# Optimization experiments

Measured on AMD Instinct MI355X. Metric: run time of the kernel, lower is better.

## Reference

```python
import jax, jax.numpy as jnp
import numpy as np

N, E, G = 40000, 400000, 64
IN, ED, HID, HEADS, OUT = 2, 18, 64, 4, 3

def _glorot(key, shape):
    fan_in = shape[0]
    return jax.random.normal(key, shape, dtype=jnp.float32) / np.float32(np.sqrt(fan_in))

def setup_inputs():
    key = jax.random.key(0)
    ks = jax.random.split(key, 32)
    d1 = HEADS * HID  # 256
    return {
        "x": jax.random.normal(ks[0], (N, IN), jnp.float32),
        "edge_index": jax.random.randint(ks[1], (2, E), 0, N),
        "edge_attr": jax.random.normal(ks[2], (E, ED), jnp.float32),
        "batch": jnp.sort(jax.random.randint(ks[3], (N,), 0, G)),
        # conv1: TransformerConv(2 -> 64, heads=4, concat=True, beta=True, edge_dim=18)
        "Wq1": _glorot(ks[4], (IN, d1)), "bq1": jnp.zeros((d1,), jnp.float32),
        "Wk1": _glorot(ks[5], (IN, d1)), "bk1": jnp.zeros((d1,), jnp.float32),
        "Wv1": _glorot(ks[6], (IN, d1)), "bv1": jnp.zeros((d1,), jnp.float32),
        "We1": _glorot(ks[7], (ED, d1)),
        "Wskip1": _glorot(ks[8], (IN, d1)), "bskip1": jnp.zeros((d1,), jnp.float32),
        "Wbeta1": _glorot(ks[9], (3 * d1, 1)),
        # conv2: TransformerConv(256 -> 64, heads=1, concat=False, beta=True, edge_dim=18)
        "Wq2": _glorot(ks[10], (d1, HID)), "bq2": jnp.zeros((HID,), jnp.float32),
        "Wk2": _glorot(ks[11], (d1, HID)), "bk2": jnp.zeros((HID,), jnp.float32),
        "Wv2": _glorot(ks[12], (d1, HID)), "bv2": jnp.zeros((HID,), jnp.float32),
        "We2": _glorot(ks[13], (ED, HID)),
        "Wskip2": _glorot(ks[14], (d1, HID)), "bskip2": jnp.zeros((HID,), jnp.float32),
        "Wbeta2": _glorot(ks[15], (3 * HID, 1)),
        "Wlin": _glorot(ks[16], (HID, OUT)), "blin": jnp.zeros((OUT,), jnp.float32),
    }

def _tconv(x, src, dst, edge_attr, Wq, bq, Wk, bk, Wv, bv, We, Wskip, bskip, Wbeta, H, C, concat):
    # PyG TransformerConv with edge_dim, beta=True, root_weight=True (eval: dropout off)
    n = x.shape[0]
    q = (x @ Wq + bq).reshape(n, H, C)
    k = (x @ Wk + bk).reshape(n, H, C)
    v = (x @ Wv + bv).reshape(n, H, C)
    e = (edge_attr @ We).reshape(-1, H, C)              # [E,H,C]
    kj = k[src] + e                                      # key_j + edge
    alpha = jnp.einsum('ehc,ehc->eh', q[dst], kj) * (1.0 / (C ** 0.5))  # [E,H]
    # segment softmax over destination nodes
    amax = jax.ops.segment_max(alpha, dst, num_segments=n)
    ex = jnp.exp(alpha - amax[dst])
    den = jax.ops.segment_sum(ex, dst, num_segments=n)
    w = ex / (den[dst] + 1e-16)
    msg = (v[src] + e) * w[:, :, None]                   # [E,H,C]
    out = jax.ops.segment_sum(msg, dst, num_segments=n)  # [N,H,C]
    out = out.reshape(n, H * C) if concat else out.mean(axis=1)
    # beta-gated skip connection
    xr = x @ Wskip + bskip
    beta = jax.nn.sigmoid(jnp.concatenate([out, xr, out - xr], axis=-1) @ Wbeta)
    return beta * xr + (1.0 - beta) * out

def reference(x, edge_index, edge_attr, batch, Wq1, bq1, Wk1, bk1, Wv1, bv1, We1, Wskip1, bskip1, Wbeta1, Wq2, bq2, Wk2, bk2, Wv2, bv2, We2, Wskip2, bskip2, Wbeta2, Wlin, blin):
    src, dst = edge_index[0], edge_index[1]
    h = jax.nn.relu(_tconv(x, src, dst, edge_attr, Wq1, bq1, Wk1, bk1, Wv1, bv1, We1, Wskip1, bskip1, Wbeta1, HEADS, HID, True))
    h = jax.nn.relu(_tconv(h, src, dst, edge_attr, Wq2, bq2, Wk2, bk2, Wv2, bv2, We2, Wskip2, bskip2, Wbeta2, 1, HID, False))
    # global mean pool per graph
    s = jax.ops.segment_sum(h, batch, num_segments=G)
    cnt = jax.ops.segment_sum(jnp.ones((h.shape[0], 1), h.dtype), batch, num_segments=G)
    pooled = s / jnp.maximum(cnt, 1.0)
    return pooled @ Wlin + blin
```

## Files before the change

### kernel.cpp

```cpp
#include <hip/hip_runtime.h>
#include <hip/hip_fp16.h>

#define N_NODES 40000
#define N_EDGES 400000
#define N_GRAPHS 64
#define D1 256
#define HIDC 64
#define NHEADS 4
#define EDIM 18
#define EPAD 20
#define OUTF 3

typedef _Float16 f16x8 __attribute__((ext_vector_type(8)));
typedef float f32x4 __attribute__((ext_vector_type(4)));

__global__ void init0(float* __restrict__ acc1, float* __restrict__ acc2,
                      float* __restrict__ out2, int* __restrict__ deg,
                      float* __restrict__ pooled, int* __restrict__ gs,
                      int* __restrict__ ge) {
    int t = blockIdx.x * 256 + threadIdx.x;
    acc1[t] = 0.f;
    if (t < N_NODES * 64) out2[t] = 0.f;
    if (t < N_NODES * 20) acc2[t] = 0.f;
    if (t < N_NODES) deg[t] = 0;
    if (t < N_GRAPHS * HIDC) pooled[t] = 0.f;
    if (t < N_GRAPHS) { gs[t] = 0; ge[t] = 0; }
}

__global__ void precompute1(const float* __restrict__ Wq, const float* __restrict__ bq,
                            const float* __restrict__ Wk, const float* __restrict__ bk,
                            const float* __restrict__ We, float* __restrict__ cbuf) {
    int t = threadIdx.x;
    if (t < 36) {
        int h = t / 9, r = t % 9, a = r / 3, b = r % 3;
        const float* A = (a == 0) ? Wq : (a == 1) ? Wq + D1 : bq;
        const float* B = (b == 0) ? Wk : (b == 1) ? Wk + D1 : bk;
        float s = 0.f;
        for (int c = 0; c < 64; ++c) s += A[h * 64 + c] * B[h * 64 + c];
        cbuf[h * 63 + a * 3 + b] = s;
    } else if (t < 252) {
        int i = t - 36;
        int h = i / 54, rr = (i % 54) / 18, j = i % 18;
        const float* A = (rr == 0) ? Wq : (rr == 1) ? Wq + D1 : bq;
        float s = 0.f;
        for (int c = 0; c < 64; ++c) s += A[h * 64 + c] * We[j * D1 + h * 64 + c];
        cbuf[h * 63 + 9 + rr * 18 + j] = s;
    }
}

__global__ void wqe_kernel(const float* __restrict__ Wq2, const float* __restrict__ bq2,
                           const float* __restrict__ We2, float* __restrict__ Wqe,
                           float* __restrict__ bias) {
    int t = blockIdx.x * 256 + threadIdx.x;
    int k = t >> 5, j = t & 31;
    float s = 0.f;
    if (j < EDIM)
        for (int c = 0; c < 64; ++c) s += Wq2[k * 64 + c] * We2[j * 64 + c];
    Wqe[k * 32 + j] = s;
    if (k == 0) {
        float b = 0.f;
        if (j < EDIM)
            for (int c = 0; c < 64; ++c) b += bq2[c] * We2[j * 64 + c];
        bias[256 + j] = b;
    }
}

__global__ void convert_w2(const float* __restrict__ Wq, const float* __restrict__ bq,
                           const float* __restrict__ Wk, const float* __restrict__ bk,
                           const float* __restrict__ Wv, const float* __restrict__ bv,
                           const float* __restrict__ Ws, const float* __restrict__ bs,
                           const float* __restrict__ Wqe,
                           __half* __restrict__ Bt, float* __restrict__ bias) {
    int t = blockIdx.x * 256 + threadIdx.x;
    int c = t >> 8, k = t & 255;
    if (c < 256) {
        int m = c >> 6, d = c & 63;
        const float* W = (m == 0) ? Wq : (m == 1) ? Wk : (m == 2) ? Wv : Ws;
        Bt[t] = __float2half(W[k * 64 + d]);
        if (k == 0) {
            const float* b = (m == 0) ? bq : (m == 1) ? bk : (m == 2) ? bv : bs;
            bias[c] = b[d];
        }
    } else {
        Bt[t] = __float2half(Wqe[k * 32 + (c - 256)]);
    }
}

__global__ void hist_kernel(const int* __restrict__ ei, int* __restrict__ deg) {
    int e = blockIdx.x * 256 + threadIdx.x;
    if (e < N_EDGES) atomicAdd(&deg[ei[N_EDGES + e]], 1);
}

__global__ void scanA(const int* __restrict__ deg, int* __restrict__ bsum) {
    __shared__ int s[256];
    int b = blockIdx.x, t = threadIdx.x;
    s[t] = (t < 160) ? deg[b * 160 + t] : 0;
    __syncthreads();
    for (int off = 128; off; off >>= 1) {
        if (t < off) s[t] += s[t + off];
        __syncthreads();
    }
    if (t == 0) bsum[b] = s[0];
}

__global__ void scanB(const int* __restrict__ bsum, int* __restrict__ boff) {
    __shared__ int s[256];
    int t = threadIdx.x;
    int v = (t < 250) ? bsum[t] : 0;
    s[t] = v;
    __syncthreads();
    for (int off = 1; off < 256; off <<= 1) {
        int add = (t >= off) ? s[t - off] : 0;
        __syncthreads();
        s[t] += add;
        __syncthreads();
    }
    if (t < 250) boff[t] = s[t] - v;
}

__global__ void scanC(const int* __restrict__ deg, const int* __restrict__ boff,
                      int* __restrict__ cursor) {
    __shared__ int s[256];
    int b = blockIdx.x, t = threadIdx.x;
    int v = (t < 160) ? deg[b * 160 + t] : 0;
    s[t] = v;
    __syncthreads();
    for (int off = 1; off < 256; off <<= 1) {
        int add = (t >= off) ? s[t - off] : 0;
        __syncthreads();
        s[t] += add;
        __syncthreads();
    }
    if (t < 160) cursor[b * 160 + t] = boff[b] + s[t] - v;
}

__global__ void perm_kernel(const int* __restrict__ ei, int* __restrict__ cursor,
                            int* __restrict__ inv) {
    int e = blockIdx.x * 256 + threadIdx.x;
    if (e >= N_EDGES) return;
    int p = atomicAdd(&cursor[ei[N_EDGES + e]], 1);
    inv[p] = e;
}

__global__ void gatherE(const int* __restrict__ inv, const int* __restrict__ ei,
                        const float* __restrict__ ea, const float* __restrict__ x,
                        const float* __restrict__ coef,
                        int* __restrict__ src_s, int* __restrict__ dst_s,
                        float* __restrict__ ea_s, float* __restrict__ alpha1) {
    int p = blockIdx.x * 256 + threadIdx.x;
    if (p >= N_EDGES) return;
    int e = inv[p];
    int src = ei[e], dst = ei[N_EDGES + e];
    src_s[p] = src;
    dst_s[p] = dst;
    const float* srow = ea + (size_t)e * EDIM;
    float s[EDIM];
    #pragma unroll
    for (int j = 0; j < EDIM; ++j) s[j] = srow[j];
    float x0 = x[src * 2], x1 = x[src * 2 + 1];
    float4* drow = (float4*)(ea_s + (size_t)p * EPAD);
    drow[0] = make_float4(s[0],  s[1],  s[2],  s[3]);
    drow[1] = make_float4(s[4],  s[5],  s[6],  s[7]);
    drow[2] = make_float4(s[8],  s[9],  s[10], s[11]);
    drow[3] = make_float4(s[12], s[13], s[14], s[15]);
    drow[4] = make_float4(s[16], s[17], x0, x1);
    const float* cb = coef + (size_t)dst * 84;
    #pragma unroll
    for (int h = 0; h < NHEADS; ++h) {
        const float* c = cb + h * 21;
        float a = x0 * c[0] + x1 * c[1] + c[2];
        #pragma unroll
        for (int j = 0; j < EDIM; ++j) a += s[j] * c[3 + j];
        alpha1[(size_t)h * N_EDGES + p] = __expf(a * 0.125f);
    }
}

__global__ void coef1(const float* __restrict__ x, const float* __restrict__ cbuf,
                      float* __restrict__ coef) {
    int t = blockIdx.x * 256 + threadIdx.x;
    int n = t / 84, r = t % 84, h = r / 21, c = r % 21;
    const float* cb = cbuf + h * 63;
    float x0 = x[2 * n], x1 = x[2 * n + 1], o;
    if (c < 3) o = x0 * cb[c] + x1 * cb[3 + c] + cb[6 + c];
    else { int j = c - 3; o = x0 * cb[9 + j] + x1 * cb[27 + j] + cb[45 + j]; }
    coef[t] = o;
}

__global__ void strip1(const int* __restrict__ dst_s, const float* __restrict__ alpha1,
                       const float* __restrict__ ea_s, float* __restrict__ acc1) {
    int t = threadIdx.x;
    int strip = blockIdx.x * 2 + (t >> 7);
    int gl = t & 127;
    bool active = gl < 84;
    int cgl = active ? gl : 83;
    int h = cgl / 21, comp = cgl % 21;
    int voff = (comp == 0) ? 18 : (comp == 1) ? 19 : (comp - 3);
    bool isone = (comp == 2);
    int p0 = strip * 16;
    int dsts[16]; float w[16]; float v[16];
    #pragma unroll
    for (int j = 0; j < 16; ++j) dsts[j] = dst_s[p0 + j];
    #pragma unroll
    for (int j = 0; j < 16; ++j) w[j] = alpha1[(size_t)h * N_EDGES + p0 + j];
    #pragma unroll
    for (int j = 0; j < 16; ++j) v[j] = isone ? 1.f : ea_s[(size_t)(p0 + j) * EPAD + voff];
    float acc = 0.f;
    int prev = dsts[0];
    #pragma unroll
    for (int j = 0; j < 16; ++j) {
        if (dsts[j] != prev) {
            if (active) atomicAdd(&acc1[(size_t)prev * 84 + gl], acc);
            acc = 0.f; prev = dsts[j];
        }
        acc += w[j] * v[j];
    }
    if (active) atomicAdd(&acc1[(size_t)prev * 84 + gl], acc);
}

__global__ void finalize1x(const float* __restrict__ x, const float* __restrict__ acc1,
                           const float* __restrict__ Wv, const float* __restrict__ bv,
                           const float* __restrict__ We, const float* __restrict__ Wskip,
                           const float* __restrict__ bskip, const float* __restrict__ Wbeta,
                           __half* __restrict__ h1f) {
    __shared__ float red[4][4];
    int nb = blockIdx.x * 4;
    int t = threadIdx.x;
    int h = t >> 6;
    float wv0 = Wv[t], wv1 = Wv[D1 + t], bvv = bv[t];
    float we[EDIM];
    #pragma unroll
    for (int j = 0; j < EDIM; ++j) we[j] = We[j * D1 + t];
    float ws0 = Wskip[t], ws1 = Wskip[D1 + t], bsv = bskip[t];
    float wb0 = Wbeta[t], wb1 = Wbeta[D1 + t], wb2 = Wbeta[2 * D1 + t];
    float o[4], xr[4], part[4];
    #pragma unroll
    for (int i = 0; i < 4; ++i) {
        int node = nb + i;
        const float* a = acc1 + (size_t)node * 84 + h * 21;
        float l = a[2];
        float oo = a[0] * wv0 + a[1] * wv1 + l * bvv;
        #pragma unroll
        for (int j = 0; j < EDIM; ++j) oo += a[3 + j] * we[j];
        oo /= (l + 1e-16f);
        float x0 = x[node * 2], x1 = x[node * 2 + 1];
        xr[i] = x0 * ws0 + x1 * ws1 + bsv;
        o[i] = oo;
        part[i] = oo * wb0 + xr[i] * wb1 + (oo - xr[i]) * wb2;
    }
    #pragma unroll
    for (int off = 32; off; off >>= 1) {
        #pragma unroll
        for (int i = 0; i < 4; ++i) part[i] += __shfl_xor(part[i], off);
    }
    if ((t & 63) == 0) {
        #pragma unroll
        for (int i = 0; i < 4; ++i) red[h][i] = part[i];
    }
    __syncthreads();
    #pragma unroll
    for (int i = 0; i < 4; ++i) {
        float tot = red[0][i] + red[1][i] + red[2][i] + red[3][i];
        float beta = 1.f / (1.f + __expf(-tot));
        h1f[(size_t)(nb + i) * D1 + t] =
            __float2half(fmaxf(beta * xr[i] + (1.f - beta) * o[i], 0.f));
    }
}

__device__ __forceinline__ void nl2_store(int c, int gr, float v,
        float* __restrict__ q2, float* __restrict__ k2, __half* __restrict__ v2h,
        float* __restrict__ xr2, float* __restrict__ qe) {
    if (c < 256) {
        int m = c >> 6, d = c & 63;
        if (m == 0)      q2[(size_t)gr * 64 + d] = v;
        else if (m == 1) k2[(size_t)gr * 64 + d] = v;
        else if (m == 2) v2h[(size_t)gr * 64 + d] = __float2half(v);
        else             xr2[(size_t)gr * 64 + d] = v;
    } else {
        qe[(size_t)gr * 32 + (c - 256)] = v;
    }
}

__global__ __launch_bounds__(256) void nl2_mfma(
        const __half* __restrict__ h1f, const __half* __restrict__ Bt,
        const float* __restrict__ bias,
        float* __restrict__ q2, float* __restrict__ k2,
        __half* __restrict__ v2h, float* __restrict__ xr2,
        float* __restrict__ qe) {
    int wave = threadIdx.x >> 6, lane = threadIdx.x & 63;
    int quad = lane >> 4, mm = lane & 15;
    int row0 = blockIdx.x * 16;
    const _Float16* Ap = (const _Float16*)h1f;
    const _Float16* Bp = (const _Float16*)Bt;
    f16x8 a[8];
    const _Float16* arow = Ap + (size_t)(row0 + mm) * 256 + quad * 8;
    #pragma unroll
    for (int s = 0; s < 8; ++s) a[s] = *(const f16x8*)(arow + s * 32);
    for (int t = wave; t < 18; t += 4) {
        int c0 = t * 16 + mm;
        const _Float16* b0 = Bp + (size_t)c0 * 256 + quad * 8;
        float bz = bias[c0];
        f32x4 accA = {bz, bz, bz, bz};
        f32x4 accB = {0.f, 0.f, 0.f, 0.f};
        #pragma unroll
        for (int s = 0; s < 4; ++s) {
            f16x8 fb0 = *(const f16x8*)(b0 + s * 32);
            f16x8 fb1 = *(const f16x8*)(b0 + (s + 4) * 32);
            accA = __builtin_amdgcn_mfma_f32_16x16x32_f16(a[s],     fb0, accA, 0, 0, 0);
            accB = __builtin_amdgcn_mfma_f32_16x16x32_f16(a[s + 4], fb1, accB, 0, 0, 0);
        }
        #pragma unroll
        for (int r = 0; r < 4; ++r) {
            int gr = row0 + quad * 4 + r;
            nl2_store(c0, gr, accA[r] + accB[r], q2, k2, v2h, xr2, qe);
        }
    }
}

#define LG2_BLOCKS 2048
#define LG2_WAVES (LG2_BLOCKS * 4)
__global__ void logits2(const int* __restrict__ src_s, const int* __restrict__ dst_s,
                        const float* __restrict__ ea_s, const float* __restrict__ q2,
                        const float* __restrict__ k2, const float* __restrict__ qe,
                        float* __restrict__ alpha2) {
    int t = threadIdx.x, wid = t >> 6, lane = t & 63;
    int w = blockIdx.x * 4 + wid;
    for (int base = w; base < N_EDGES; base += 2 * LG2_WAVES) {
        int p1 = base, p2 = base + LG2_WAVES;
        bool has2 = p2 < N_EDGES;
        int p2c = has2 ? p2 : p1;
        int s1 = src_s[p1], d1 = dst_s[p1];
        int s2 = src_s[p2c], d2 = dst_s[p2c];
        float dd1 = q2[(size_t)d1 * 64 + lane] * k2[(size_t)s1 * 64 + lane];
        float dd2 = q2[(size_t)d2 * 64 + lane] * k2[(size_t)s2 * 64 + lane];
        if (lane < 20) {
            dd1 += qe[(size_t)d1 * 32 + lane] * ea_s[(size_t)p1 * EPAD + lane];
            dd2 += qe[(size_t)d2 * 32 + lane] * ea_s[(size_t)p2c * EPAD + lane];
        }
        #pragma unroll
        for (int off = 32; off; off >>= 1) {
            dd1 += __shfl_xor(dd1, off);
            dd2 += __shfl_xor(dd2, off);
        }
        if (lane == 0) {
            alpha2[p1] = __expf(dd1 * 0.125f);
            if (has2) alpha2[p2] = __expf(dd2 * 0.125f);
        }
    }
}

__global__ void spmm2s(const int* __restrict__ dst_s, const int* __restrict__ src_s,
                       const float* __restrict__ alpha2, const __half* __restrict__ v2h,
                       const float* __restrict__ ea_s,
                       float* __restrict__ out2, float* __restrict__ acc2) {
    int t = threadIdx.x;
    int strip = blockIdx.x * 4 + (t >> 6);
    int lane = t & 63;
    int p0 = strip * 16;
    int dsts[16]; int srcs[16]; float w[16];
    #pragma unroll
    for (int j = 0; j < 16; ++j) dsts[j] = dst_s[p0 + j];
    #pragma unroll
    for (int j = 0; j < 16; ++j) srcs[j] = src_s[p0 + j];
    #pragma unroll
    for (int j = 0; j < 16; ++j) w[j] = alpha2[p0 + j];
    float vv[16]; float ev[16];
    #pragma unroll
    for (int j = 0; j < 16; ++j) vv[j] = __half2float(v2h[(size_t)srcs[j] * 64 + lane]);
    #pragma unroll
    for (int j = 0; j < 16; ++j)
        ev[j] = (lane < EDIM) ? ea_s[(size_t)(p0 + j) * EPAD + lane] : 1.f;
    float acc = 0.f, accS = 0.f;
    int prev = dsts[0];
    #pragma unroll
    for (int j = 0; j < 16; ++j) {
        if (dsts[j] != prev) {
            atomicAdd(&out2[(size_t)prev * 64 + lane], acc);
            if (lane < 19) atomicAdd(&acc2[(size_t)prev * 20 + lane], accS);
            acc = 0.f; accS = 0.f; prev = dsts[j];
        }
        acc += w[j] * vv[j];
        accS += w[j] * ev[j];
    }
    atomicAdd(&out2[(size_t)prev * 64 + lane], acc);
    if (lane < 19) atomicAdd(&acc2[(size_t)prev * 20 + lane], accS);
}

__global__ void finalize2x(const float* __restrict__ out2, const float* __restrict__ acc2,
                           const float* __restrict__ xr2, const float* __restrict__ We2,
                           const float* __restrict__ Wb2, float* __restrict__ h2) {
    __shared__ float w2s[EDIM * 64];
    int t = threadIdx.x;
    for (int i = t; i < EDIM * 64; i += 256) w2s[i] = We2[i];
    __syncthreads();
    int node = blockIdx.x * 4 + (t >> 6);
    int lane = t & 63;
    const float* a2 = acc2 + (size_t)node * 20;
    float num = out2[(size_t)node * 64 + lane];
    #pragma unroll
    for (int j = 0; j < EDIM; ++j) num += a2[j] * w2s[j * 64 + lane];
    float o = num / (a2[18] + 1e-16f);
    float xr = xr2[(size_t)node * 64 + lane];
    float part = o * Wb2[lane] + xr * Wb2[64 + lane] + (o - xr) * Wb2[128 + lane];
    #pragma unroll
    for (int off = 32; off; off >>= 1) part += __shfl_xor(part, off);
    float beta = 1.f / (1.f + __expf(-part));
    h2[(size_t)node * 64 + lane] = fmaxf(beta * xr + (1.f - beta) * o, 0.f);
}

__global__ void bounds_kernel(const int* __restrict__ batch, int* __restrict__ gs,
                              int* __restrict__ ge) {
    int n = blockIdx.x * 256 + threadIdx.x;
    if (n >= N_NODES) return;
    int b = batch[n];
    if (n == 0) gs[b] = 0;
    else { int pb = batch[n - 1]; if (pb != b) { ge[pb] = n; gs[b] = n; } }
    if (n == N_NODES - 1) ge[b] = N_NODES;
}

__global__ void pool_kernel(const float* __restrict__ h2, const int* __restrict__ gs,
                            const int* __restrict__ ge, float* __restrict__ pooled,
                            float* __restrict__ cnt) {
    __shared__ float red[4][64];
    int g = blockIdx.x >> 2, q = blockIdx.x & 3;
    int t = threadIdx.x, wv = t >> 6, lane = t & 63;
    int s = gs[g], e = ge[g];
    float sum = 0.f;
    for (int n = s + q * 4 + wv; n < e; n += 16) sum += h2[(size_t)n * 64 + lane];
    red[wv][lane] = sum;
    __syncthreads();
    if (wv == 0) {
        float v = red[0][lane] + red[1][lane] + red[2][lane] + red[3][lane];
        atomicAdd(&pooled[g * 64 + lane], v);
    }
    if (q == 0 && t == 0) cnt[g] = (float)(e - s);
}

__global__ void final_lin(const float* __restrict__ pooled, const float* __restrict__ cnt,
                          const float* __restrict__ Wlin, const float* __restrict__ blin,
                          float* __restrict__ out) {
    int t = threadIdx.x;
    if (t >= N_GRAPHS * OUTF) return;
    int g = t / OUTF, o = t % OUTF;
    float inv = 1.f / fmaxf(cnt[g], 1.f);
    float acc = 0.f;
    for (int kk = 0; kk < HIDC; ++kk) acc += pooled[g * 64 + kk] * Wlin[kk * OUTF + o];
    out[t] = acc * inv + blin[o];
}

extern "C" void kernel_launch(void* const* d_in, const int* in_sizes, int n_in,
                              void* d_out, int out_size, void* d_ws, size_t ws_size,
                              hipStream_t stream) {
    const float* x      = (const float*)d_in[0];
    const int*   ei     = (const int*)d_in[1];
    const float* ea     = (const float*)d_in[2];
    const int*   batch  = (const int*)d_in[3];
    const float* Wq1    = (const float*)d_in[4];  const float* bq1    = (const float*)d_in[5];
    const float* Wk1    = (const float*)d_in[6];  const float* bk1    = (const float*)d_in[7];
    const float* Wv1    = (const float*)d_in[8];  const float* bv1    = (const float*)d_in[9];
    const float* We1    = (const float*)d_in[10];
    const float* Wskip1 = (const float*)d_in[11]; const float* bskip1 = (const float*)d_in[12];
    const float* Wbeta1 = (const float*)d_in[13];
    const float* Wq2    = (const float*)d_in[14]; const float* bq2    = (const float*)d_in[15];
    const float* Wk2    = (const float*)d_in[16]; const float* bk2    = (const float*)d_in[17];
    const float* Wv2    = (const float*)d_in[18]; const float* bv2    = (const float*)d_in[19];
    const float* We2    = (const float*)d_in[20];
    const float* Wskip2 = (const float*)d_in[21]; const float* bskip2 = (const float*)d_in[22];
    const float* Wbeta2 = (const float*)d_in[23];
    const float* Wlin   = (const float*)d_in[24]; const float* blin   = (const float*)d_in[25];

    float* ptr = (float*)d_ws;
    float* q2     = ptr; ptr += (size_t)N_NODES * 64;
    float* k2     = ptr; ptr += (size_t)N_NODES * 64;
    float* xr2    = ptr; ptr += (size_t)N_NODES * 64;
    float* qe     = ptr; ptr += (size_t)N_NODES * 32;
    __half* v2h   = (__half*)ptr; ptr += (size_t)N_NODES * 32;
    float* ea_s   = ptr; ptr += (size_t)N_EDGES * EPAD;
    float* alpha2 = ptr; ptr += N_EDGES;
    float* acc2   = ptr; ptr += (size_t)N_NODES * 20;
    float* out2   = ptr; ptr += (size_t)N_NODES * 64;
    float* pooled = ptr; ptr += N_GRAPHS * HIDC;
    float* cnt    = ptr; ptr += N_GRAPHS;
    int*   gs     = (int*)ptr; ptr += N_GRAPHS;
    int*   ge     = (int*)ptr; ptr += N_GRAPHS;
    float* cbuf   = ptr; ptr += 256;
    float* bias   = ptr; ptr += 320;
    float* Wqe    = ptr; ptr += 256 * 32;
    __half* Bt    = (__half*)ptr; ptr += (288 * 256) / 2;
    int*   src_s  = (int*)ptr; ptr += N_EDGES;
    int*   dst_s  = (int*)ptr; ptr += N_EDGES;
    int*   inv    = (int*)ptr; ptr += N_EDGES;
    int*   deg    = (int*)ptr; ptr += N_NODES;
    int*   cursor = (int*)ptr; ptr += N_NODES;
    int*   bsum   = (int*)ptr; ptr += 256;
    int*   boff   = (int*)ptr; ptr += 256;
    float* coef   = ptr; ptr += (size_t)N_NODES * 84;
    float* h2     = coef;
    float* acc1   = ptr; ptr += (size_t)N_NODES * 84;
    float* alpha1 = ptr; ptr += (size_t)4 * N_EDGES;
    __half* h1f   = (__half*)ptr; ptr += (size_t)N_NODES * 128;

    const int EB = (N_EDGES + 255) / 256;
    const int NB = (N_NODES + 255) / 256;

    init0<<<(N_NODES * 84) / 256, 256, 0, stream>>>(acc1, acc2, out2, deg, pooled, gs, ge);
    precompute1<<<1, 256, 0, stream>>>(Wq1, bq1, Wk1, bk1, We1, cbuf);
    coef1<<<(N_NODES * 84) / 256, 256, 0, stream>>>(x, cbuf, coef);
    wqe_kernel<<<32, 256, 0, stream>>>(Wq2, bq2, We2, Wqe, bias);
    convert_w2<<<288, 256, 0, stream>>>(Wq2, bq2, Wk2, bk2, Wv2, bv2, Wskip2, bskip2,
                                        Wqe, Bt, bias);
    hist_kernel<<<EB, 256, 0, stream>>>(ei, deg);
    scanA<<<250, 256, 0, stream>>>(deg, bsum);
    scanB<<<1, 256, 0, stream>>>(bsum, boff);
    scanC<<<250, 256, 0, stream>>>(deg, boff, cursor);
    perm_kernel<<<EB, 256, 0, stream>>>(ei, cursor, inv);
    gatherE<<<EB, 256, 0, stream>>>(inv, ei, ea, x, coef, src_s, dst_s, ea_s, alpha1);

    strip1<<<(N_EDGES / 16) / 2, 256, 0, stream>>>(dst_s, alpha1, ea_s, acc1);
    finalize1x<<<N_NODES / 4, 256, 0, stream>>>(x, acc1, Wv1, bv1, We1, Wskip1, bskip1,
                                                Wbeta1, h1f);

    nl2_mfma<<<N_NODES / 16, 256, 0, stream>>>(h1f, Bt, bias, q2, k2, v2h, xr2, qe);
    logits2<<<LG2_BLOCKS, 256, 0, stream>>>(src_s, dst_s, ea_s, q2, k2, qe, alpha2);
    spmm2s<<<(N_EDGES / 16) / 4, 256, 0, stream>>>(dst_s, src_s, alpha2, v2h, ea_s,
                                                   out2, acc2);
    finalize2x<<<N_NODES / 4, 256, 0, stream>>>(out2, acc2, xr2, We2, Wbeta2, h2);

    bounds_kernel<<<NB, 256, 0, stream>>>(batch, gs, ge);
    pool_kernel<<<N_GRAPHS * 4, 256, 0, stream>>>(h2, gs, ge, pooled, cnt);
    final_lin<<<1, 256, 0, stream>>>(pooled, cnt, Wlin, blin, (float*)d_out);
}
```

Baseline: 459.6 us.

## Fuse weight-prep kernels and restructure layer-2 MFMA GEMM to keep B in registers

Merges precompute1, wqe_kernel and convert_w2 into a single prep_w launch, writing Wq2·We2 straight into the fp16 B matrix without the Wqe intermediate, and folds coef1 into the init kernel. This cuts five small launches down to two. The layer-2 MFMA GEMM is also remapped so each wave owns one 16-column tile and holds its B fragments in registers while looping over 8 row tiles, instead of reloading B for every row block. The trade-off is that the same A rows are now read by 18 different waves through cache instead of being loaded once per block.

Measured after the change: 449.8 us. 1.02x faster.

```diff
diff --git a/kernel.cpp b/kernel.cpp
--- a/kernel.cpp
+++ b/kernel.cpp
@@ -14,76 +14,77 @@
 typedef _Float16 f16x8 __attribute__((ext_vector_type(8)));
 typedef float f32x4 __attribute__((ext_vector_type(4)));
 
-__global__ void init0(float* __restrict__ acc1, float* __restrict__ acc2,
-                      float* __restrict__ out2, int* __restrict__ deg,
-                      float* __restrict__ pooled, int* __restrict__ gs,
-                      int* __restrict__ ge) {
+__global__ void prep_w(const float* __restrict__ Wq, const float* __restrict__ bq,
+                       const float* __restrict__ Wk, const float* __restrict__ bk,
+                       const float* __restrict__ Wv, const float* __restrict__ bv,
+                       const float* __restrict__ Ws, const float* __restrict__ bs,
+                       const float* __restrict__ We2,
+                       const float* __restrict__ Wq1, const float* __restrict__ bq1,
+                       const float* __restrict__ Wk1, const float* __restrict__ bk1,
+                       const float* __restrict__ We1,
+                       __half* __restrict__ Bt, float* __restrict__ bias,
+                       float* __restrict__ cbuf) {
+    int c = blockIdx.x, k = threadIdx.x;
+    if (c < 256) {
+        int m = c >> 6, d = c & 63;
+        const float* W = (m == 0) ? Wq : (m == 1) ? Wk : (m == 2) ? Wv : Ws;
+        Bt[c * 256 + k] = __float2half(W[k * 64 + d]);
+        if (k == 0) {
+            const float* b = (m == 0) ? bq : (m == 1) ? bk : (m == 2) ? bv : bs;
+            bias[c] = b[d];
+        }
+    } else if (c < 288) {
+        int j = c - 256;
+        float s = 0.f;
+        if (j < EDIM)
+            for (int cc = 0; cc < 64; ++cc) s += Wq[k * 64 + cc] * We2[j * 64 + cc];
+        Bt[c * 256 + k] = __float2half(s);
+        if (k == 0) {
+            float b = 0.f;
+            if (j < EDIM)
+                for (int cc = 0; cc < 64; ++cc) b += bq[cc] * We2[j * 64 + cc];
+            bias[c] = b;
+        }
+    } else {
+        int t = k;
+        if (t < 36) {
+            int h = t / 9, r = t % 9, a = r / 3, b = r % 3;
+            const float* A = (a == 0) ? Wq1 : (a == 1) ? Wq1 + D1 : bq1;
+            const float* B = (b == 0) ? Wk1 : (b == 1) ? Wk1 + D1 : bk1;
+            float s = 0.f;
+            for (int cc = 0; cc < 64; ++cc) s += A[h * 64 + cc] * B[h * 64 + cc];
+            cbuf[h * 63 + a * 3 + b] = s;
+        } else if (t < 252) {
+            int i = t - 36;
+            int h = i / 54, rr = (i % 54) / 18, j = i % 18;
+            const float* A = (rr == 0) ? Wq1 : (rr == 1) ? Wq1 + D1 : bq1;
+            float s = 0.f;
+            for (int cc = 0; cc < 64; ++cc) s += A[h * 64 + cc] * We1[j * D1 + h * 64 + cc];
+            cbuf[h * 63 + 9 + rr * 18 + j] = s;
+        }
+    }
+}
+
+__global__ void initA(const float* __restrict__ x, const float* __restrict__ cbuf,
+                      float* __restrict__ coef, float* __restrict__ acc1,
+                      float* __restrict__ acc2, float* __restrict__ out2,
+                      int* __restrict__ deg, float* __restrict__ pooled,
+                      int* __restrict__ gs, int* __restrict__ ge) {
     int t = blockIdx.x * 256 + threadIdx.x;
     acc1[t] = 0.f;
+    {
+        int n = t / 84, r = t % 84, h = r / 21, c = r % 21;
+        const float* cb = cbuf + h * 63;
+        float x0 = x[2 * n], x1 = x[2 * n + 1], o;
+        if (c < 3) o = x0 * cb[c] + x1 * cb[3 + c] + cb[6 + c];
+        else { int j = c - 3; o = x0 * cb[9 + j] + x1 * cb[27 + j] + cb[45 + j]; }
+        coef[t] = o;
+    }
     if (t < N_NODES * 64) out2[t] = 0.f;
     if (t < N_NODES * 20) acc2[t] = 0.f;
     if (t < N_NODES) deg[t] = 0;
     if (t < N_GRAPHS * HIDC) pooled[t] = 0.f;
     if (t < N_GRAPHS) { gs[t] = 0; ge[t] = 0; }
-}
-
-__global__ void precompute1(const float* __restrict__ Wq, const float* __restrict__ bq,
-                            const float* __restrict__ Wk, const float* __restrict__ bk,
-                            const float* __restrict__ We, float* __restrict__ cbuf) {
-    int t = threadIdx.x;
-    if (t < 36) {
-        int h = t / 9, r = t % 9, a = r / 3, b = r % 3;
-        const float* A = (a == 0) ? Wq : (a == 1) ? Wq + D1 : bq;
-        const float* B = (b == 0) ? Wk : (b == 1) ? Wk + D1 : bk;
-        float s = 0.f;
-        for (int c = 0; c < 64; ++c) s += A[h * 64 + c] * B[h * 64 + c];
-        cbuf[h * 63 + a * 3 + b] = s;
-    } else if (t < 252) {
-        int i = t - 36;
-        int h = i / 54, rr = (i % 54) / 18, j = i % 18;
-        const float* A = (rr == 0) ? Wq : (rr == 1) ? Wq + D1 : bq;
-        float s = 0.f;
-        for (int c = 0; c < 64; ++c) s += A[h * 64 + c] * We[j * D1 + h * 64 + c];
-        cbuf[h * 63 + 9 + rr * 18 + j] = s;
-    }
-}
-
-__global__ void wqe_kernel(const float* __restrict__ Wq2, const float* __restrict__ bq2,
-                           const float* __restrict__ We2, float* __restrict__ Wqe,
-                           float* __restrict__ bias) {
-    int t = blockIdx.x * 256 + threadIdx.x;
-    int k = t >> 5, j = t & 31;
-    float s = 0.f;
-    if (j < EDIM)
-        for (int c = 0; c < 64; ++c) s += Wq2[k * 64 + c] * We2[j * 64 + c];
-    Wqe[k * 32 + j] = s;
-    if (k == 0) {
-        float b = 0.f;
-        if (j < EDIM)
-            for (int c = 0; c < 64; ++c) b += bq2[c] * We2[j * 64 + c];
-        bias[256 + j] = b;
-    }
-}
-
-__global__ void convert_w2(const float* __restrict__ Wq, const float* __restrict__ bq,
-                           const float* __restrict__ Wk, const float* __restrict__ bk,
-                           const float* __restrict__ Wv, const float* __restrict__ bv,
-                           const float* __restrict__ Ws, const float* __restrict__ bs,
-                           const float* __restrict__ Wqe,
-                           __half* __restrict__ Bt, float* __restrict__ bias) {
-    int t = blockIdx.x * 256 + threadIdx.x;
-    int c = t >> 8, k = t & 255;
-    if (c < 256) {
-        int m = c >> 6, d = c & 63;
-        const float* W = (m == 0) ? Wq : (m == 1) ? Wk : (m == 2) ? Wv : Ws;
-        Bt[t] = __float2half(W[k * 64 + d]);
-        if (k == 0) {
-            const float* b = (m == 0) ? bq : (m == 1) ? bk : (m == 2) ? bv : bs;
-            bias[c] = b[d];
-        }
-    } else {
-        Bt[t] = __float2half(Wqe[k * 32 + (c - 256)]);
-    }
 }
 
 __global__ void hist_kernel(const int* __restrict__ ei, int* __restrict__ deg) {
@@ -175,17 +176,6 @@
     }
 }
 
-__global__ void coef1(const float* __restrict__ x, const float* __restrict__ cbuf,
-                      float* __restrict__ coef) {
-    int t = blockIdx.x * 256 + threadIdx.x;
-    int n = t / 84, r = t % 84, h = r / 21, c = r % 21;
-    const float* cb = cbuf + h * 63;
-    float x0 = x[2 * n], x1 = x[2 * n + 1], o;
-    if (c < 3) o = x0 * cb[c] + x1 * cb[3 + c] + cb[6 + c];
-    else { int j = c - 3; o = x0 * cb[9 + j] + x1 * cb[27 + j] + cb[45 + j]; }
-    coef[t] = o;
-}
-
 __global__ void strip1(const int* __restrict__ dst_s, const float* __restrict__ alpha1,
                        const float* __restrict__ ea_s, float* __restrict__ acc1) {
     int t = threadIdx.x;
@@ -286,27 +276,31 @@
         float* __restrict__ q2, float* __restrict__ k2,
         __half* __restrict__ v2h, float* __restrict__ xr2,
         float* __restrict__ qe) {
-    int wave = threadIdx.x >> 6, lane = threadIdx.x & 63;
-    int quad = lane >> 4, mm = lane & 15;
-    int row0 = blockIdx.x * 16;
+    int W = blockIdx.x * 4 + (threadIdx.x >> 6);
+    if (W >= 18 * 313) return;
+    int ct = W % 18, chunk = W / 18;
+    int lane = threadIdx.x & 63, quad = lane >> 4, mm = lane & 15;
+    int c0 = ct * 16 + mm;
     const _Float16* Ap = (const _Float16*)h1f;
     const _Float16* Bp = (const _Float16*)Bt;
-    f16x8 a[8];
-    const _Float16* arow = Ap + (size_t)(row0 + mm) * 256 + quad * 8;
-    #pragma unroll
-    for (int s = 0; s < 8; ++s) a[s] = *(const f16x8*)(arow + s * 32);
-    for (int t = wave; t < 18; t += 4) {
-        int c0 = t * 16 + mm;
-        const _Float16* b0 = Bp + (size_t)c0 * 256 + quad * 8;
-        float bz = bias[c0];
+    const _Float16* b0 = Bp + (size_t)c0 * 256 + quad * 8;
+    f16x8 b[8];
+    #pragma unroll
+    for (int s = 0; s < 8; ++s) b[s] = *(const f16x8*)(b0 + s * 32);
+    float bz = bias[c0];
+    int rt_end = chunk * 8 + 8; if (rt_end > 2500) rt_end = 2500;
+    for (int rt = chunk * 8; rt < rt_end; ++rt) {
+        int row0 = rt * 16;
+        const _Float16* arow = Ap + (size_t)(row0 + mm) * 256 + quad * 8;
+        f16x8 a[8];
+        #pragma unroll
+        for (int s = 0; s < 8; ++s) a[s] = *(const f16x8*)(arow + s * 32);
         f32x4 accA = {bz, bz, bz, bz};
         f32x4 accB = {0.f, 0.f, 0.f, 0.f};
         #pragma unroll
         for (int s = 0; s < 4; ++s) {
-            f16x8 fb0 = *(const f16x8*)(b0 + s * 32);
-            f16x8 fb1 = *(const f16x8*)(b0 + (s + 4) * 32);
-            accA = __builtin_amdgcn_mfma_f32_16x16x32_f16(a[s],     fb0, accA, 0, 0, 0);
-            accB = __builtin_amdgcn_mfma_f32_16x16x32_f16(a[s + 4], fb1, accB, 0, 0, 0);
+            accA = __builtin_amdgcn_mfma_f32_16x16x32_f16(a[s],     b[s],     accA, 0, 0, 0);
+            accB = __builtin_amdgcn_mfma_f32_16x16x32_f16(a[s + 4], b[s + 4], accB, 0, 0, 0);
         }
         #pragma unroll
         for (int r = 0; r < 4; ++r) {
@@ -484,7 +478,6 @@
     int*   ge     = (int*)ptr; ptr += N_GRAPHS;
     float* cbuf   = ptr; ptr += 256;
     float* bias   = ptr; ptr += 320;
-    float* Wqe    = ptr; ptr += 256 * 32;
     __half* Bt    = (__half*)ptr; ptr += (288 * 256) / 2;
     int*   src_s  = (int*)ptr; ptr += N_EDGES;
     int*   dst_s  = (int*)ptr; ptr += N_EDGES;
@@ -502,12 +495,10 @@
     const int EB = (N_EDGES + 255) / 256;
     const int NB = (N_NODES + 255) / 256;
 
-    init0<<<(N_NODES * 84) / 256, 256, 0, stream>>>(acc1, acc2, out2, deg, pooled, gs, ge);
-    precompute1<<<1, 256, 0, stream>>>(Wq1, bq1, Wk1, bk1, We1, cbuf);
-    coef1<<<(N_NODES * 84) / 256, 256, 0, stream>>>(x, cbuf, coef);
-    wqe_kernel<<<32, 256, 0, stream>>>(Wq2, bq2, We2, Wqe, bias);
-    convert_w2<<<288, 256, 0, stream>>>(Wq2, bq2, Wk2, bk2, Wv2, bv2, Wskip2, bskip2,
-                                        Wqe, Bt, bias);
+    prep_w<<<289, 256, 0, stream>>>(Wq2, bq2, Wk2, bk2, Wv2, bv2, Wskip2, bskip2, We2,
+                                    Wq1, bq1, Wk1, bk1, We1, Bt, bias, cbuf);
+    initA<<<(N_NODES * 84) / 256, 256, 0, stream>>>(x, cbuf, coef, acc1, acc2, out2,
+                                                    deg, pooled, gs, ge);
     hist_kernel<<<EB, 256, 0, stream>>>(ei, deg);
     scanA<<<250, 256, 0, stream>>>(deg, bsum);
     scanB<<<1, 256, 0, stream>>>(bsum, boff);
@@ -519,7 +510,7 @@
     finalize1x<<<N_NODES / 4, 256, 0, stream>>>(x, acc1, Wv1, bv1, We1, Wskip1, bskip1,
                                                 Wbeta1, h1f);
 
-    nl2_mfma<<<N_NODES / 16, 256, 0, stream>>>(h1f, Bt, bias, q2, k2, v2h, xr2, qe);
+    nl2_mfma<<<1409, 256, 0, stream>>>(h1f, Bt, bias, q2, k2, v2h, xr2, qe);
     logits2<<<LG2_BLOCKS, 256, 0, stream>>>(src_s, dst_s, ea_s, q2, k2, qe, alpha2);
     spmm2s<<<(N_EDGES / 16) / 4, 256, 0, stream>>>(dst_s, src_s, alpha2, v2h, ea_s,
                                                    out2, acc2);
```
